# Performance work log

Hardware: AMD Instinct MI355X
Metric: run time of the kernel (lower is better)

The kernel has to match this reference:

```python
import jax, jax.numpy as jnp
import numpy as np

B, S, D, H = 128, 4096, 64, 256  # num_mlps, tokens per MLP, d_model, d_hidden


def setup_inputs() -> dict:
    key = jax.random.key(0)
    kx, k1, k2 = jax.random.split(key, 3)
    x = jax.random.normal(kx, (B, S, D), dtype=jnp.float32)
    # Stacked per-MLP weights (one 2-layer SiLU MLP per batch index, no bias)
    W1 = jax.random.normal(k1, (B, D, H), dtype=jnp.float32) * (1.0 / np.sqrt(D))
    W2 = jax.random.normal(k2, (B, H, D), dtype=jnp.float32) * (1.0 / np.sqrt(H))
    return {"x": x, "W1": W1, "W2": W2}


def reference(x, W1, W2):
    # outputs[i] = mlp_i(x[i]); stacked + residual -> one batched GEMM pair
    h = jax.nn.silu(jnp.einsum('bsd,bdh->bsh', x, W1))  # [B,S,H]
    out = jnp.einsum('bsh,bhd->bsd', h, W2)             # [B,S,D]
    return out + x
```

## Files before the change

kernel.cpp:

```cpp
#include <hip/hip_runtime.h>
#include <stdint.h>

#define BB 128
#define SS 4096
#define DD 64
#define HH 256

typedef short bf16x8 __attribute__((ext_vector_type(8)));
typedef float f32x16 __attribute__((ext_vector_type(16)));
typedef float f32x2 __attribute__((ext_vector_type(2)));

__device__ __forceinline__ uint32_t cvt_pk_bf16(float lo, float hi) {
  uint32_t r;
  asm("v_cvt_pk_bf16_f32 %0, %1, %2" : "=v"(r) : "v"(lo), "v"(hi));
  return r;
}

__device__ __forceinline__ void permswap(uint32_t& a, uint32_t& b) {
  asm("v_permlane32_swap_b32 %0, %1" : "+v"(a), "+v"(b));
}

__device__ __forceinline__ uint32_t silu2_pack(float a, float b) {
  f32x2 v = {a, b};
  f32x2 m = v * (-1.44269504f);
  float ea, eb;
  asm("v_exp_f32 %0, %1" : "=v"(ea) : "v"(m.x));
  asm("v_exp_f32 %0, %1" : "=v"(eb) : "v"(m.y));
  f32x2 d = {ea, eb};
  d = d + (f32x2){1.0f, 1.0f};
  f32x2 r = {__builtin_amdgcn_rcpf(d.x), __builtin_amdgcn_rcpf(d.y)};
  f32x2 o = v * r;
  return cvt_pk_bf16(o.x, o.y);
}

__device__ __forceinline__ void gload16(const void* g, void* l) {
  __builtin_amdgcn_global_load_lds(
      (const __attribute__((address_space(1))) void*)g,
      (__attribute__((address_space(3))) void*)l, 16, 0, 0);
}

__global__ __launch_bounds__(256) void transpose_w(
    const float* __restrict__ W1, const float* __restrict__ W2,
    ushort* __restrict__ W1f, ushort* __restrict__ W2f) {
  int g = blockIdx.x * 256 + threadIdx.x;
  const int half = (BB * DD * HH) / 8;
  float v[8];
  if (g < half) {
    size_t e = (size_t)g * 8;
    int b = (int)(e >> 14);
    int rem = (int)(e & 16383);
    int tile = rem >> 9;
    int lane6 = (rem >> 3) & 63;
    int hc = tile >> 2, kc = tile & 3;
    int h = hc * 32 + (lane6 & 31);
    int d0 = kc * 16 + (lane6 >> 5) * 8;
    const float* src = W1 + ((size_t)b << 14) + h;
#pragma unroll
    for (int j = 0; j < 8; ++j) v[j] = src[(size_t)(d0 + j) << 8];
    uint4 o;
    o.x = cvt_pk_bf16(v[0], v[1]); o.y = cvt_pk_bf16(v[2], v[3]);
    o.z = cvt_pk_bf16(v[4], v[5]); o.w = cvt_pk_bf16(v[6], v[7]);
    *reinterpret_cast<uint4*>(W1f + e) = o;
  } else if (g < 2 * half) {
    size_t e = (size_t)(g - half) * 8;
    int b = (int)(e >> 14);
    int rem = (int)(e & 16383);
    int tile = rem >> 9;
    int lane6 = (rem >> 3) & 63;
    int hc = tile >> 2, mt = (tile >> 1) & 1, c = tile & 1;
    int d = mt * 32 + (lane6 & 31);
    int h0 = hc * 32 + c * 16 + (lane6 >> 5) * 8;
    const float* src = W2 + ((size_t)b << 14) + d;
#pragma unroll
    for (int j = 0; j < 8; ++j) v[j] = src[(size_t)(h0 + j) << 6];
    uint4 o;
    o.x = cvt_pk_bf16(v[0], v[1]); o.y = cvt_pk_bf16(v[2], v[3]);
    o.z = cvt_pk_bf16(v[4], v[5]); o.w = cvt_pk_bf16(v[6], v[7]);
    *reinterpret_cast<uint4*>(W2f + e) = o;
  }
}

__global__ __launch_bounds__(512, 4) void mlp_fused(
    const float* __restrict__ xg, const ushort* __restrict__ w1f,
    const ushort* __restrict__ w2f, float* __restrict__ outg) {
  __shared__ int4 lds4[65536 / 16];
  char* lds = (char*)lds4;

  const int tid = threadIdx.x;
  const int wave = tid >> 6;
  const int lane = tid & 63;
  const int l31 = lane & 31;
  const int g5 = lane >> 5;

  int raw = blockIdx.x;
  int logical = (raw & 7) * 256 + (raw >> 3);
  const int b = logical >> 4;
  const int st = logical & 15;
  const int s_base = st * 256 + wave * 32;

  const float* xb = xg + (((size_t)b * SS + s_base) << 6);
  const char* w1b = (const char*)(w1f + ((size_t)b << 14));
  const char* w2b = (const char*)(w2f + ((size_t)b << 14));

#pragma unroll
  for (int r = 0; r < 4; ++r) {
    uint32_t o = (uint32_t)(r * 8192 + tid * 16);
    gload16(w1b + o, lds + o);
    gload16(w2b + o, lds + 32768 + o);
  }

  bf16x8 bx[4];
#pragma unroll
  for (int kc = 0; kc < 4; ++kc) {
    const float* p = xb + ((size_t)l31 << 6) + kc * 16 + g5 * 8;
    float4 fa = *reinterpret_cast<const float4*>(p);
    float4 fb = *reinterpret_cast<const float4*>(p + 4);
    union { uint32_t u[4]; bf16x8 v; } cv;
    cv.u[0] = cvt_pk_bf16(fa.x, fa.y);
    cv.u[1] = cvt_pk_bf16(fa.z, fa.w);
    cv.u[2] = cvt_pk_bf16(fb.x, fb.y);
    cv.u[3] = cvt_pk_bf16(fb.z, fb.w);
    bx[kc] = cv.v;
  }

  f32x16 acc[2];
  {
    const float* prow = xb + ((size_t)l31 << 6);
#pragma unroll
    for (int mt = 0; mt < 2; ++mt)
#pragma unroll
      for (int q = 0; q < 4; ++q) {
        float4 v =
            *reinterpret_cast<const float4*>(prow + mt * 32 + q * 8 + g5 * 4);
        acc[mt][4 * q + 0] = v.x;
        acc[mt][4 * q + 1] = v.y;
        acc[mt][4 * q + 2] = v.z;
        acc[mt][4 * q + 3] = v.w;
      }
  }

  __syncthreads();

  const char* lw1 = lds + lane * 16;
  const char* lw2 = lds + 32768 + lane * 16;

  const f32x16 vzero = {0.f, 0.f, 0.f, 0.f, 0.f, 0.f, 0.f, 0.f,
                        0.f, 0.f, 0.f, 0.f, 0.f, 0.f, 0.f, 0.f};

#pragma unroll
  for (int hc = 0; hc < 8; ++hc) {
    bf16x8 a1[4];
#pragma unroll
    for (int kc = 0; kc < 4; ++kc)
      a1[kc] = *reinterpret_cast<const bf16x8*>(lw1 + (hc * 4 + kc) * 1024);
    f32x16 ah0 = vzero, ah1 = vzero;
    ah0 = __builtin_amdgcn_mfma_f32_32x32x16_bf16(a1[0], bx[0], ah0, 0, 0, 0);
    ah1 = __builtin_amdgcn_mfma_f32_32x32x16_bf16(a1[1], bx[1], ah1, 0, 0, 0);
    ah0 = __builtin_amdgcn_mfma_f32_32x32x16_bf16(a1[2], bx[2], ah0, 0, 0, 0);
    ah1 = __builtin_amdgcn_mfma_f32_32x32x16_bf16(a1[3], bx[3], ah1, 0, 0, 0);
    f32x16 ah = ah0 + ah1;

    bf16x8 bh[2];
#pragma unroll
    for (int c = 0; c < 2; ++c) {
      uint32_t A0 = silu2_pack(ah[8 * c + 0], ah[8 * c + 1]);
      uint32_t A1 = silu2_pack(ah[8 * c + 2], ah[8 * c + 3]);
      uint32_t B0 = silu2_pack(ah[8 * c + 4], ah[8 * c + 5]);
      uint32_t B1 = silu2_pack(ah[8 * c + 6], ah[8 * c + 7]);
      permswap(A0, B0);
      permswap(A1, B1);
      union { uint32_t u[4]; bf16x8 v; } f;
      f.u[0] = A0; f.u[1] = A1; f.u[2] = B0; f.u[3] = B1;
      bh[c] = f.v;
    }

#pragma unroll
    for (int c = 0; c < 2; ++c)
#pragma unroll
      for (int mt = 0; mt < 2; ++mt) {
        bf16x8 a2 = *reinterpret_cast<const bf16x8*>(
            lw2 + (hc * 4 + mt * 2 + c) * 1024);
        acc[mt] =
            __builtin_amdgcn_mfma_f32_32x32x16_bf16(a2, bh[c], acc[mt], 0, 0, 0);
      }
  }

  float* prow = outg + (((size_t)b * SS + s_base + l31) << 6);
#pragma unroll
  for (int mt = 0; mt < 2; ++mt)
#pragma unroll
    for (int q = 0; q < 4; ++q) {
      float4 v;
      v.x = acc[mt][4 * q + 0];
      v.y = acc[mt][4 * q + 1];
      v.z = acc[mt][4 * q + 2];
      v.w = acc[mt][4 * q + 3];
      *reinterpret_cast<float4*>(prow + mt * 32 + q * 8 + g5 * 4) = v;
    }
}

extern "C" void kernel_launch(void* const* d_in, const int* in_sizes, int n_in,
                              void* d_out, int out_size, void* d_ws, size_t ws_size,
                              hipStream_t stream) {
  const float* x  = (const float*)d_in[0];
  const float* W1 = (const float*)d_in[1];
  const float* W2 = (const float*)d_in[2];
  float* out = (float*)d_out;

  ushort* W1f = (ushort*)d_ws;
  ushort* W2f = W1f + (size_t)BB * DD * HH;

  transpose_w<<<2048, 256, 0, stream>>>(W1, W2, W1f, W2f);
  mlp_fused<<<2048, 512, 0, stream>>>(x, W1f, W2f, out);
}
```

Measured before the change: 85.51 us.

## Stage x loads and output stores through swizzled LDS for coalesced global access

The block's x tile is now loaded with fully coalesced float4 reads, converted to bf16 and written to a swizzled LDS region. The MFMA B fragments and the residual accumulator init are then read back from LDS. After the MLP, accumulators are written to per-wave swizzled LDS slices and stored to global as contiguous rows. The W2 load now reuses the x region, so it waits for x staging behind extra barriers, and the layer-1 MFMAs run as one dependent accumulator chain instead of two. The residual now uses bf16-rounded x instead of fp32 x, which adds numerical error.

Result: faster. 78.90 us (median of 2 runs) (-7.7%).

```diff
diff --git a/kernel.cpp b/kernel.cpp
--- a/kernel.cpp
+++ b/kernel.cpp
@@ -14,6 +14,13 @@
   uint32_t r;
   asm("v_cvt_pk_bf16_f32 %0, %1, %2" : "=v"(r) : "v"(lo), "v"(hi));
   return r;
+}
+
+__device__ __forceinline__ float bflo(uint32_t w) {
+  union { uint32_t u; float f; } c; c.u = w << 16; return c.f;
+}
+__device__ __forceinline__ float bfhi(uint32_t w) {
+  union { uint32_t u; float f; } c; c.u = w & 0xffff0000u; return c.f;
 }
 
 __device__ __forceinline__ void permswap(uint32_t& a, uint32_t& b) {
@@ -98,67 +105,82 @@
   const int st = logical & 15;
   const int s_base = st * 256 + wave * 32;
 
-  const float* xb = xg + (((size_t)b * SS + s_base) << 6);
   const char* w1b = (const char*)(w1f + ((size_t)b << 14));
   const char* w2b = (const char*)(w2f + ((size_t)b << 14));
+  char* xlds = lds + 32768;
 
 #pragma unroll
   for (int r = 0; r < 4; ++r) {
     uint32_t o = (uint32_t)(r * 8192 + tid * 16);
     gload16(w1b + o, lds + o);
-    gload16(w2b + o, lds + 32768 + o);
-  }
+  }
+
+  const float* xblk = xg + (((size_t)b * SS + st * 256) << 6);
+#pragma unroll
+  for (int ps = 0; ps < 4; ++ps) {
+    int e = ps * 4096 + tid * 8;
+    float4 fa = *reinterpret_cast<const float4*>(xblk + e);
+    float4 fb = *reinterpret_cast<const float4*>(xblk + e + 4);
+    uint4 pk;
+    pk.x = cvt_pk_bf16(fa.x, fa.y);
+    pk.y = cvt_pk_bf16(fa.z, fa.w);
+    pk.z = cvt_pk_bf16(fb.x, fb.y);
+    pk.w = cvt_pk_bf16(fb.z, fb.w);
+    int row = e >> 6, d0 = e & 63;
+    uint32_t byte = (uint32_t)(row * 128 + d0 * 2);
+    byte ^= (uint32_t)(row & 7) << 4;
+    *reinterpret_cast<uint4*>(xlds + byte) = pk;
+  }
+
+  __syncthreads();
+
+  const int R = wave * 32 + l31;
+  const uint32_t rs = (uint32_t)(R & 7) << 4;
 
   bf16x8 bx[4];
 #pragma unroll
   for (int kc = 0; kc < 4; ++kc) {
-    const float* p = xb + ((size_t)l31 << 6) + kc * 16 + g5 * 8;
-    float4 fa = *reinterpret_cast<const float4*>(p);
-    float4 fb = *reinterpret_cast<const float4*>(p + 4);
-    union { uint32_t u[4]; bf16x8 v; } cv;
-    cv.u[0] = cvt_pk_bf16(fa.x, fa.y);
-    cv.u[1] = cvt_pk_bf16(fa.z, fa.w);
-    cv.u[2] = cvt_pk_bf16(fb.x, fb.y);
-    cv.u[3] = cvt_pk_bf16(fb.z, fb.w);
-    bx[kc] = cv.v;
+    uint32_t byte = (uint32_t)(R * 128 + kc * 32 + g5 * 16) ^ rs;
+    bx[kc] = *reinterpret_cast<const bf16x8*>(xlds + byte);
   }
 
   f32x16 acc[2];
-  {
-    const float* prow = xb + ((size_t)l31 << 6);
-#pragma unroll
-    for (int mt = 0; mt < 2; ++mt)
-#pragma unroll
-      for (int q = 0; q < 4; ++q) {
-        float4 v =
-            *reinterpret_cast<const float4*>(prow + mt * 32 + q * 8 + g5 * 4);
-        acc[mt][4 * q + 0] = v.x;
-        acc[mt][4 * q + 1] = v.y;
-        acc[mt][4 * q + 2] = v.z;
-        acc[mt][4 * q + 3] = v.w;
-      }
+#pragma unroll
+  for (int mt = 0; mt < 2; ++mt)
+#pragma unroll
+    for (int q = 0; q < 4; ++q) {
+      uint32_t byte = (uint32_t)(R * 128 + mt * 64 + q * 16 + g5 * 8) ^ rs;
+      uint2 w = *reinterpret_cast<const uint2*>(xlds + byte);
+      acc[mt][4 * q + 0] = bflo(w.x);
+      acc[mt][4 * q + 1] = bfhi(w.x);
+      acc[mt][4 * q + 2] = bflo(w.y);
+      acc[mt][4 * q + 3] = bfhi(w.y);
+    }
+
+  __syncthreads();
+
+#pragma unroll
+  for (int r = 0; r < 4; ++r) {
+    uint32_t o = (uint32_t)(r * 8192 + tid * 16);
+    gload16(w2b + o, xlds + o);
   }
 
   __syncthreads();
 
   const char* lw1 = lds + lane * 16;
-  const char* lw2 = lds + 32768 + lane * 16;
+  const char* lw2 = xlds + lane * 16;
 
   const f32x16 vzero = {0.f, 0.f, 0.f, 0.f, 0.f, 0.f, 0.f, 0.f,
                         0.f, 0.f, 0.f, 0.f, 0.f, 0.f, 0.f, 0.f};
 
 #pragma unroll
   for (int hc = 0; hc < 8; ++hc) {
-    bf16x8 a1[4];
-#pragma unroll
-    for (int kc = 0; kc < 4; ++kc)
-      a1[kc] = *reinterpret_cast<const bf16x8*>(lw1 + (hc * 4 + kc) * 1024);
-    f32x16 ah0 = vzero, ah1 = vzero;
-    ah0 = __builtin_amdgcn_mfma_f32_32x32x16_bf16(a1[0], bx[0], ah0, 0, 0, 0);
-    ah1 = __builtin_amdgcn_mfma_f32_32x32x16_bf16(a1[1], bx[1], ah1, 0, 0, 0);
-    ah0 = __builtin_amdgcn_mfma_f32_32x32x16_bf16(a1[2], bx[2], ah0, 0, 0, 0);
-    ah1 = __builtin_amdgcn_mfma_f32_32x32x16_bf16(a1[3], bx[3], ah1, 0, 0, 0);
-    f32x16 ah = ah0 + ah1;
+    f32x16 ah = vzero;
+#pragma unroll
+    for (int kc = 0; kc < 4; ++kc) {
+      bf16x8 a1 = *reinterpret_cast<const bf16x8*>(lw1 + (hc * 4 + kc) * 1024);
+      ah = __builtin_amdgcn_mfma_f32_32x32x16_bf16(a1, bx[kc], ah, 0, 0, 0);
+    }
 
     bf16x8 bh[2];
 #pragma unroll
@@ -185,18 +207,38 @@
       }
   }
 
-  float* prow = outg + (((size_t)b * SS + s_base + l31) << 6);
-#pragma unroll
-  for (int mt = 0; mt < 2; ++mt)
-#pragma unroll
-    for (int q = 0; q < 4; ++q) {
-      float4 v;
-      v.x = acc[mt][4 * q + 0];
-      v.y = acc[mt][4 * q + 1];
-      v.z = acc[mt][4 * q + 2];
-      v.w = acc[mt][4 * q + 3];
-      *reinterpret_cast<float4*>(prow + mt * 32 + q * 8 + g5 * 4) = v;
-    }
+  __syncthreads();
+
+  char* slice = lds + wave * 8192;
+  {
+    uint32_t sw = (uint32_t)(l31 & 7) << 4;
+#pragma unroll
+    for (int mt = 0; mt < 2; ++mt)
+#pragma unroll
+      for (int q = 0; q < 4; ++q) {
+        uint32_t byte =
+            ((uint32_t)(l31 * 256 + mt * 128 + q * 32 + g5 * 16)) ^ sw;
+        float4 v;
+        v.x = acc[mt][4 * q + 0];
+        v.y = acc[mt][4 * q + 1];
+        v.z = acc[mt][4 * q + 2];
+        v.w = acc[mt][4 * q + 3];
+        *reinterpret_cast<float4*>(slice + byte) = v;
+      }
+  }
+  __builtin_amdgcn_sched_barrier(0);
+  {
+    float* orow = outg + (((size_t)b * SS + s_base) << 6);
+#pragma unroll
+    for (int it = 0; it < 8; ++it) {
+      uint32_t o = (uint32_t)(it * 1024 + lane * 16);
+      uint32_t row = o >> 8;
+      uint32_t byte = o ^ ((row & 7) << 4);
+      float4 v = *reinterpret_cast<const float4*>(slice + byte);
+      *reinterpret_cast<float4*>(orow + ((size_t)row << 6) + ((o & 255) >> 2)) =
+          v;
+    }
+  }
 }
 
 extern "C" void kernel_launch(void* const* d_in, const int* in_sizes, int n_in,
```
